# Kernel tuning notes

Measured on AMD Instinct MI355X. Metric: run time of the kernel, lower is better.

The kernel has to match this reference:

```python
import jax, jax.numpy as jnp
import numpy as np

W_IMPORTANCE = 0.1  # from __init__ default
EPS = 1e-12         # F.normalize eps


def _l2norm(x):
    n = jnp.sqrt(jnp.sum(x * x, axis=1, keepdims=True))
    return x / jnp.maximum(n, EPS)


def setup_inputs() -> dict:
    key = jax.random.key(0)
    k1, k2, k3 = jax.random.split(key, 3)
    return {
        "target_edge_feats": jax.random.normal(k1, (16384, 512), dtype=jnp.float32),
        "source_edge_feats": jax.random.normal(k2, (32768, 512), dtype=jnp.float32),
        "source_importance": jax.random.uniform(k3, (32768,), dtype=jnp.float32),
        "topk": 8,
        "chunk_size": 4096,
    }


def reference(target_edge_feats, source_edge_feats, source_importance, topk, chunk_size):
    E_t, Fdim = target_edge_feats.shape
    tn = _l2norm(target_edge_feats)            # [E_t, F]
    sn = _l2norm(source_edge_feats)            # [E_s, F]
    bias = W_IMPORTANCE * source_importance    # [E_s]

    n_chunks = E_t // chunk_size               # E_t chosen as exact multiple
    t_chunks = tn.reshape(n_chunks, chunk_size, Fdim)

    def per_chunk(t):
        # cosine similarity + importance bias, then top-k over sources
        score = jnp.einsum('cf,ef->ce', t, sn) + bias[None, :]  # [chunk, E_s]
        vals, idx = jax.lax.top_k(score, topk)
        return vals, idx

    vals, idx = jax.lax.map(per_chunk, t_chunks)  # [n_chunks, chunk, K]
    topk_score = vals.reshape(E_t, topk)
    topk_idx = idx.reshape(E_t, topk)
    topk_alpha = jax.nn.softmax(topk_score, axis=-1)
    return (topk_idx, topk_score, topk_alpha)
```

## Files before the change

### kernel.cpp

```cpp
#include <hip/hip_runtime.h>
#include <hip/hip_bf16.h>
#include <float.h>

#define KDIM 512
#define MBLK 64
#define NBLK 256
#define KBLK 32
#define NTH  256
#define APAD 68
#define BPAD 260
#define TOPK 8

__device__ __forceinline__ float bf16_rne_f32(float v) {
  return __bfloat162float(__float2bfloat16(v));
}

__global__ void er_norms(const float* __restrict__ T, const float* __restrict__ S,
                         float* __restrict__ nt, float* __restrict__ ns,
                         int M, int N) {
  int gid = blockIdx.x * blockDim.x + threadIdx.x;
  int row = gid >> 2;
  int b   = gid & 3;
  if (row >= M + N) return;
  const float* base = (row < M) ? (T + (size_t)row * KDIM)
                                : (S + (size_t)(row - M) * KDIM);
  const float4* p4 = (const float4*)(base + b * 128);
  float r[8];
  {
    float4 f0 = p4[0], f1 = p4[1];
    r[0] = __fmul_rn(f0.x, f0.x); r[1] = __fmul_rn(f0.y, f0.y);
    r[2] = __fmul_rn(f0.z, f0.z); r[3] = __fmul_rn(f0.w, f0.w);
    r[4] = __fmul_rn(f1.x, f1.x); r[5] = __fmul_rn(f1.y, f1.y);
    r[6] = __fmul_rn(f1.z, f1.z); r[7] = __fmul_rn(f1.w, f1.w);
  }
  #pragma unroll
  for (int i = 2; i < 32; i += 2) {
    float4 f0 = p4[i], f1 = p4[i + 1];
    r[0] = __fadd_rn(r[0], __fmul_rn(f0.x, f0.x));
    r[1] = __fadd_rn(r[1], __fmul_rn(f0.y, f0.y));
    r[2] = __fadd_rn(r[2], __fmul_rn(f0.z, f0.z));
    r[3] = __fadd_rn(r[3], __fmul_rn(f0.w, f0.w));
    r[4] = __fadd_rn(r[4], __fmul_rn(f1.x, f1.x));
    r[5] = __fadd_rn(r[5], __fmul_rn(f1.y, f1.y));
    r[6] = __fadd_rn(r[6], __fmul_rn(f1.z, f1.z));
    r[7] = __fadd_rn(r[7], __fmul_rn(f1.w, f1.w));
  }
  float B = __fadd_rn(__fadd_rn(__fadd_rn(r[0], r[1]), __fadd_rn(r[2], r[3])),
                      __fadd_rn(__fadd_rn(r[4], r[5]), __fadd_rn(r[6], r[7])));
  float t = __fadd_rn(B, __shfl_xor(B, 1, 64));
  float s = __fadd_rn(t, __shfl_xor(t, 2, 64));
  if (b == 0) {
    float nr = __fsqrt_rn(s);
    if (row < M) nt[row] = nr; else ns[row - M] = nr;
  }
}

__global__ __launch_bounds__(NTH, 1)
void er_fused(const float* __restrict__ A, const float* __restrict__ B,
              const float* __restrict__ imp,
              const float* __restrict__ nt, const float* __restrict__ ns,
              float* __restrict__ out, int M, int N) {
  __shared__ float a_lds[KBLK][APAD];
  __shared__ float b_lds[KBLK][BPAD];
  __shared__ float tval[MBLK][TOPK];
  __shared__ int   tidx[MBLK][TOPK];
  __shared__ float tthr[MBLK];

  const int tid    = threadIdx.x;
  const int m_base = blockIdx.x * MBLK;
  const int tm = tid >> 5;
  const int tn = tid & 31;
  const int lane = tid & 63;
  const int ntiles = N / NBLK;

  if (tid < MBLK) {
    tthr[tid] = -FLT_MAX;
    #pragma unroll
    for (int j = 0; j < TOPK; ++j) { tval[tid][j] = -FLT_MAX; tidx[tid][j] = 0; }
  }
  __syncthreads();

  #pragma unroll 1
  for (int t = 0; t < ntiles; ++t) {
    const int n_base = t * NBLK;
    float acc[8][8];
    #pragma unroll
    for (int i = 0; i < 8; ++i)
      #pragma unroll
      for (int j = 0; j < 8; ++j) acc[i][j] = 0.f;

    float4 ar[2], br[8];
    #pragma unroll
    for (int ii = 0; ii < 2; ++ii) {
      int u = tid + NTH * ii, row = u >> 3, ks = u & 7;
      ar[ii] = *(const float4*)&A[(size_t)(m_base + row) * KDIM + ks * 4];
    }
    #pragma unroll
    for (int ii = 0; ii < 8; ++ii) {
      int u = tid + NTH * ii, row = u >> 3, ks = u & 7;
      br[ii] = *(const float4*)&B[(size_t)(n_base + row) * KDIM + ks * 4];
    }

    #pragma unroll 1
    for (int kc = 0; kc < KDIM / KBLK; ++kc) {
      __syncthreads();
      #pragma unroll
      for (int ii = 0; ii < 2; ++ii) {
        int u = tid + NTH * ii, row = u >> 3, ks = u & 7;
        float dn = fmaxf(nt[m_base + row], 1e-12f);
        a_lds[ks*4+0][row] = __fdiv_rn(ar[ii].x, dn);
        a_lds[ks*4+1][row] = __fdiv_rn(ar[ii].y, dn);
        a_lds[ks*4+2][row] = __fdiv_rn(ar[ii].z, dn);
        a_lds[ks*4+3][row] = __fdiv_rn(ar[ii].w, dn);
      }
      #pragma unroll
      for (int ii = 0; ii < 8; ++ii) {
        int u = tid + NTH * ii, row = u >> 3, ks = u & 7;
        float dn = fmaxf(ns[n_base + row], 1e-12f);
        b_lds[ks*4+0][row] = __fdiv_rn(br[ii].x, dn);
        b_lds[ks*4+1][row] = __fdiv_rn(br[ii].y, dn);
        b_lds[ks*4+2][row] = __fdiv_rn(br[ii].z, dn);
        b_lds[ks*4+3][row] = __fdiv_rn(br[ii].w, dn);
      }
      __syncthreads();
      if (kc + 1 < KDIM / KBLK) {
        int kb = (kc + 1) * KBLK;
        #pragma unroll
        for (int ii = 0; ii < 2; ++ii) {
          int u = tid + NTH * ii, row = u >> 3, ks = u & 7;
          ar[ii] = *(const float4*)&A[(size_t)(m_base + row) * KDIM + kb + ks * 4];
        }
        #pragma unroll
        for (int ii = 0; ii < 8; ++ii) {
          int u = tid + NTH * ii, row = u >> 3, ks = u & 7;
          br[ii] = *(const float4*)&B[(size_t)(n_base + row) * KDIM + kb + ks * 4];
        }
      }
      #pragma unroll 8
      for (int k = 0; k < KBLK; ++k) {
        const float4* ap = (const float4*)&a_lds[k][tm * 8];
        const float4* bp = (const float4*)&b_lds[k][tn * 8];
        float4 a0 = ap[0], a1 = ap[1], b0 = bp[0], b1 = bp[1];
        float av[8] = {a0.x,a0.y,a0.z,a0.w,a1.x,a1.y,a1.z,a1.w};
        float bw[8] = {b0.x,b0.y,b0.z,b0.w,b1.x,b1.y,b1.z,b1.w};
        #pragma unroll
        for (int i = 0; i < 8; ++i)
          #pragma unroll
          for (int j = 0; j < 8; ++j)
            acc[i][j] = fmaf(av[i], bw[j], acc[i][j]);
      }
    }

    float bv[8];
    #pragma unroll
    for (int j = 0; j < 8; ++j) bv[j] = __fmul_rn(0.1f, imp[n_base + tn * 8 + j]);

    int need = 0;
    #pragma unroll
    for (int i = 0; i < 8; ++i) {
      float thr = tthr[tm * 8 + i];
      #pragma unroll
      for (int j = 0; j < 8; ++j) {
        float s = __fadd_rn(acc[i][j], bv[j]);
        need |= (s > thr) ? 1 : 0;
      }
    }
    unsigned long long mask = __ballot(need);
    while (mask) {
      int cur = __ffsll(mask) - 1;
      mask &= mask - 1;
      if (lane == cur) {
        #pragma unroll
        for (int i = 0; i < 8; ++i) {
          int r = tm * 8 + i;
          #pragma unroll
          for (int j = 0; j < 8; ++j) {
            float s = __fadd_rn(acc[i][j], bv[j]);
            if (s > tthr[r]) {
              int p = TOPK - 1;
              while (p > 0 && tval[r][p-1] < s) {
                tval[r][p] = tval[r][p-1];
                tidx[r][p] = tidx[r][p-1];
                --p;
              }
              tval[r][p] = s;
              tidx[r][p] = n_base + tn * 8 + j;
              tthr[r] = tval[r][TOPK-1];
            }
          }
        }
      }
    }
  }

  __syncthreads();

  if (tid < MBLK) {
    float v[TOPK]; int id[TOPK];
    #pragma unroll
    for (int j = 0; j < TOPK; ++j) { v[j] = tval[tid][j]; id[j] = tidx[tid][j]; }
    float mx = v[0];
    float e[TOPK];
    #pragma unroll
    for (int j = 0; j < TOPK; ++j) e[j] = expf(__fadd_rn(v[j], -mx));
    float sum = __fadd_rn(
        __fadd_rn(__fadd_rn(e[0], e[1]), __fadd_rn(e[2], e[3])),
        __fadd_rn(__fadd_rn(e[4], e[5]), __fadd_rn(e[6], e[7])));
    const size_t SEC  = (size_t)M * TOPK;
    const size_t base = (size_t)(m_base + tid) * TOPK;
    #pragma unroll
    for (int j = 0; j < TOPK; ++j) {
      out[base + j]         = bf16_rne_f32((float)id[j]);
      out[SEC + base + j]   = bf16_rne_f32(v[j]);
      out[2*SEC + base + j] = bf16_rne_f32(__fdiv_rn(e[j], sum));
    }
  }
}

extern "C" void kernel_launch(void* const* d_in, const int* in_sizes, int n_in,
                              void* d_out, int out_size, void* d_ws, size_t ws_size,
                              hipStream_t stream) {
  const float* T   = (const float*)d_in[0];
  const float* S   = (const float*)d_in[1];
  const float* imp = (const float*)d_in[2];
  int M = in_sizes[0] / KDIM;
  int N = in_sizes[1] / KDIM;

  float* nt = (float*)d_ws;
  float* ns = nt + M;

  float* out = (float*)d_out;

  er_norms<<<(4 * (M + N) + 255) / 256, 256, 0, stream>>>(T, S, nt, ns, M, N);
  er_fused<<<M / MBLK, NTH, 0, stream>>>(T, S, imp, nt, ns, out, M, N);
}
```

Before: 10.79 ms.

## Split source columns across blocks with per-split top-k and merge kernel

Splits the source dimension into up to four partitions so the grid launches four times as many blocks. Each block keeps a partial top-8 per target row and writes it to workspace, and a new merge kernel combines the partials and computes the softmax. KBLK is halved and launch bounds are raised to allow more resident blocks per CU. The cost is extra workspace traffic, a third kernel launch, and possibly more global reloads of the target tile.

```diff
diff --git a/kernel.cpp b/kernel.cpp
--- a/kernel.cpp
+++ b/kernel.cpp
@@ -5,7 +5,7 @@
 #define KDIM 512
 #define MBLK 64
 #define NBLK 256
-#define KBLK 32
+#define KBLK 16
 #define NTH  256
 #define APAD 68
 #define BPAD 260
@@ -55,11 +55,12 @@
   }
 }
 
-__global__ __launch_bounds__(NTH, 1)
-void er_fused(const float* __restrict__ A, const float* __restrict__ B,
-              const float* __restrict__ imp,
-              const float* __restrict__ nt, const float* __restrict__ ns,
-              float* __restrict__ out, int M, int N) {
+__global__ __launch_bounds__(NTH, 4)
+void er_cand(const float* __restrict__ A, const float* __restrict__ B,
+             const float* __restrict__ imp,
+             const float* __restrict__ nt, const float* __restrict__ ns,
+             float* __restrict__ pval, int* __restrict__ pidx,
+             int M, int N, int nsplit, int mblocks) {
   __shared__ float a_lds[KBLK][APAD];
   __shared__ float b_lds[KBLK][BPAD];
   __shared__ float tval[MBLK][TOPK];
@@ -67,11 +68,15 @@
   __shared__ float tthr[MBLK];
 
   const int tid    = threadIdx.x;
-  const int m_base = blockIdx.x * MBLK;
+  const int mb     = blockIdx.x % mblocks;
+  const int split  = blockIdx.x / mblocks;
+  const int m_base = mb * MBLK;
+  const int n_cols = N / nsplit;
+  const int n_start = split * n_cols;
+  const int ntiles  = n_cols / NBLK;
   const int tm = tid >> 5;
   const int tn = tid & 31;
   const int lane = tid & 63;
-  const int ntiles = N / NBLK;
 
   if (tid < MBLK) {
     tthr[tid] = -FLT_MAX;
@@ -80,42 +85,39 @@
   }
   __syncthreads();
 
+  const int srow = tid >> 2;
+  const int sks  = tid & 3;
+
   #pragma unroll 1
   for (int t = 0; t < ntiles; ++t) {
-    const int n_base = t * NBLK;
+    const int n_base = n_start + t * NBLK;
     float acc[8][8];
     #pragma unroll
     for (int i = 0; i < 8; ++i)
       #pragma unroll
       for (int j = 0; j < 8; ++j) acc[i][j] = 0.f;
 
-    float4 ar[2], br[8];
-    #pragma unroll
-    for (int ii = 0; ii < 2; ++ii) {
-      int u = tid + NTH * ii, row = u >> 3, ks = u & 7;
-      ar[ii] = *(const float4*)&A[(size_t)(m_base + row) * KDIM + ks * 4];
-    }
-    #pragma unroll
-    for (int ii = 0; ii < 8; ++ii) {
-      int u = tid + NTH * ii, row = u >> 3, ks = u & 7;
+    float4 ar, br[4];
+    ar = *(const float4*)&A[(size_t)(m_base + srow) * KDIM + sks * 4];
+    #pragma unroll
+    for (int ii = 0; ii < 4; ++ii) {
+      int u = tid + NTH * ii, row = u >> 2, ks = u & 3;
       br[ii] = *(const float4*)&B[(size_t)(n_base + row) * KDIM + ks * 4];
     }
 
     #pragma unroll 1
     for (int kc = 0; kc < KDIM / KBLK; ++kc) {
       __syncthreads();
+      {
+        float dn = fmaxf(nt[m_base + srow], 1e-12f);
+        a_lds[sks*4+0][srow] = __fdiv_rn(ar.x, dn);
+        a_lds[sks*4+1][srow] = __fdiv_rn(ar.y, dn);
+        a_lds[sks*4+2][srow] = __fdiv_rn(ar.z, dn);
+        a_lds[sks*4+3][srow] = __fdiv_rn(ar.w, dn);
+      }
       #pragma unroll
-      for (int ii = 0; ii < 2; ++ii) {
-        int u = tid + NTH * ii, row = u >> 3, ks = u & 7;
-        float dn = fmaxf(nt[m_base + row], 1e-12f);
-        a_lds[ks*4+0][row] = __fdiv_rn(ar[ii].x, dn);
-        a_lds[ks*4+1][row] = __fdiv_rn(ar[ii].y, dn);
-        a_lds[ks*4+2][row] = __fdiv_rn(ar[ii].z, dn);
-        a_lds[ks*4+3][row] = __fdiv_rn(ar[ii].w, dn);
-      }
-      #pragma unroll
-      for (int ii = 0; ii < 8; ++ii) {
-        int u = tid + NTH * ii, row = u >> 3, ks = u & 7;
+      for (int ii = 0; ii < 4; ++ii) {
+        int u = tid + NTH * ii, row = u >> 2, ks = u & 3;
         float dn = fmaxf(ns[n_base + row], 1e-12f);
         b_lds[ks*4+0][row] = __fdiv_rn(br[ii].x, dn);
         b_lds[ks*4+1][row] = __fdiv_rn(br[ii].y, dn);
@@ -125,18 +127,14 @@
       __syncthreads();
       if (kc + 1 < KDIM / KBLK) {
         int kb = (kc + 1) * KBLK;
+        ar = *(const float4*)&A[(size_t)(m_base + srow) * KDIM + kb + sks * 4];
         #pragma unroll
-        for (int ii = 0; ii < 2; ++ii) {
-          int u = tid + NTH * ii, row = u >> 3, ks = u & 7;
-          ar[ii] = *(const float4*)&A[(size_t)(m_base + row) * KDIM + kb + ks * 4];
-        }
-        #pragma unroll
-        for (int ii = 0; ii < 8; ++ii) {
-          int u = tid + NTH * ii, row = u >> 3, ks = u & 7;
+        for (int ii = 0; ii < 4; ++ii) {
+          int u = tid + NTH * ii, row = u >> 2, ks = u & 3;
           br[ii] = *(const float4*)&B[(size_t)(n_base + row) * KDIM + kb + ks * 4];
         }
       }
-      #pragma unroll 8
+      #pragma unroll 16
       for (int k = 0; k < KBLK; ++k) {
         const float4* ap = (const float4*)&a_lds[k][tm * 8];
         const float4* bp = (const float4*)&b_lds[k][tn * 8];
@@ -194,26 +192,44 @@
   }
 
   __syncthreads();
-
-  if (tid < MBLK) {
-    float v[TOPK]; int id[TOPK];
-    #pragma unroll
-    for (int j = 0; j < TOPK; ++j) { v[j] = tval[tid][j]; id[j] = tidx[tid][j]; }
-    float mx = v[0];
-    float e[TOPK];
-    #pragma unroll
-    for (int j = 0; j < TOPK; ++j) e[j] = expf(__fadd_rn(v[j], -mx));
-    float sum = __fadd_rn(
-        __fadd_rn(__fadd_rn(e[0], e[1]), __fadd_rn(e[2], e[3])),
-        __fadd_rn(__fadd_rn(e[4], e[5]), __fadd_rn(e[6], e[7])));
-    const size_t SEC  = (size_t)M * TOPK;
-    const size_t base = (size_t)(m_base + tid) * TOPK;
-    #pragma unroll
-    for (int j = 0; j < TOPK; ++j) {
-      out[base + j]         = bf16_rne_f32((float)id[j]);
-      out[SEC + base + j]   = bf16_rne_f32(v[j]);
-      out[2*SEC + base + j] = bf16_rne_f32(__fdiv_rn(e[j], sum));
-    }
+  for (int r = tid; r < MBLK; r += NTH) {
+    size_t off = ((size_t)split * M + m_base + r) * TOPK;
+    #pragma unroll
+    for (int j = 0; j < TOPK; ++j) { pval[off + j] = tval[r][j]; pidx[off + j] = tidx[r][j]; }
+  }
+}
+
+__global__ void er_merge(const float* __restrict__ pval, const int* __restrict__ pidx,
+                         float* __restrict__ out, int M, int nsplit) {
+  int m = blockIdx.x * blockDim.x + threadIdx.x;
+  if (m >= M) return;
+  int heads[4] = {0, 0, 0, 0};
+  float v[TOPK]; int id[TOPK];
+  for (int o = 0; o < TOPK; ++o) {
+    float bvv = -FLT_MAX; int bi = 0x7fffffff; int bs = 0;
+    for (int s = 0; s < nsplit; ++s) {
+      if (heads[s] < TOPK) {
+        size_t off = ((size_t)s * M + m) * TOPK + heads[s];
+        float vv = pval[off]; int ii = pidx[off];
+        if (vv > bvv || (vv == bvv && ii < bi)) { bvv = vv; bi = ii; bs = s; }
+      }
+    }
+    v[o] = bvv; id[o] = bi; heads[bs]++;
+  }
+  float mx = v[0];
+  float e[TOPK];
+  #pragma unroll
+  for (int j = 0; j < TOPK; ++j) e[j] = expf(__fadd_rn(v[j], -mx));
+  float sum = __fadd_rn(
+      __fadd_rn(__fadd_rn(e[0], e[1]), __fadd_rn(e[2], e[3])),
+      __fadd_rn(__fadd_rn(e[4], e[5]), __fadd_rn(e[6], e[7])));
+  const size_t SEC  = (size_t)M * TOPK;
+  const size_t base = (size_t)m * TOPK;
+  #pragma unroll
+  for (int j = 0; j < TOPK; ++j) {
+    out[base + j]         = bf16_rne_f32((float)id[j]);
+    out[SEC + base + j]   = bf16_rne_f32(v[j]);
+    out[2*SEC + base + j] = bf16_rne_f32(__fdiv_rn(e[j], sum));
   }
 }
 
@@ -226,11 +242,22 @@
   int M = in_sizes[0] / KDIM;
   int N = in_sizes[1] / KDIM;
 
-  float* nt = (float*)d_ws;
-  float* ns = nt + M;
-
-  float* out = (float*)d_out;
-
+  int nsplit = 4;
+  while (nsplit > 1) {
+    size_t need = (size_t)(M + N) * 4 + (size_t)nsplit * M * TOPK * 8;
+    if (need <= ws_size) break;
+    nsplit >>= 1;
+  }
+
+  float* nt   = (float*)d_ws;
+  float* ns   = nt + M;
+  float* pval = ns + N;
+  int*   pidx = (int*)(pval + (size_t)nsplit * M * TOPK);
+  float* out  = (float*)d_out;
+
+  int mblocks = M / MBLK;
   er_norms<<<(4 * (M + N) + 255) / 256, 256, 0, stream>>>(T, S, nt, ns, M, N);
-  er_fused<<<M / MBLK, NTH, 0, stream>>>(T, S, imp, nt, ns, out, M, N);
-}
+  er_cand<<<mblocks * nsplit, NTH, 0, stream>>>(T, S, imp, nt, ns,
+                                                pval, pidx, M, N, nsplit, mblocks);
+  er_merge<<<(M + 255) / 256, 256, 0, stream>>>(pval, pidx, out, M, nsplit);
+}
```

New measurement: 16.22 ms. 1.5x slower.
